# Performance work log

Hardware: AMD Instinct MI355X
Metric: run time of the kernel (lower is better)

The kernel has to match this reference:

```python
import jax, jax.numpy as jnp
import numpy as np

N, E, IN_DIM, HID, K, EXP_HID = 50000, 800000, 128, 64, 4, 64


def _xavier(key, shape):
    fan_in, fan_out = shape[-2], shape[-1]
    lim = np.sqrt(6.0 / (fan_in + fan_out)).astype(np.float32)
    return jax.random.uniform(key, shape, jnp.float32, -lim, lim)


def setup_inputs() -> dict:
    key = jax.random.key(0)
    ks = jax.random.split(key, 6)
    return {
        "x": jax.random.normal(ks[0], (N, IN_DIM), jnp.float32),
        "edge_index": jax.random.randint(ks[1], (2, E), 0, N),
        # InitDisenLayer: K per-channel Linear(IN_DIM -> HID)
        "W_init": _xavier(ks[2], (K, IN_DIM, HID)),
        "b_init": jnp.zeros((K, HID), jnp.float32),
        # elayers: Linear(2*HID -> EXP_HID) -> ReLU -> Linear(EXP_HID -> 1)
        "W1": _xavier(ks[3], (2 * HID, EXP_HID)),
        "b1": jnp.zeros((EXP_HID,), jnp.float32),
        "W2": _xavier(ks[4], (EXP_HID, 1)),
        "b2": jnp.zeros((1,), jnp.float32),
    }


def reference(x, edge_index, W_init, b_init, W1, b1, W2, b2):
    # InitDisenLayer: per-channel linear -> relu -> l2-normalize => Z [N, K, HID]
    Z = jax.nn.relu(jnp.einsum('ni,kih->nkh', x, W_init) + b_init)
    Z = Z / jnp.maximum(jnp.linalg.norm(Z, axis=-1, keepdims=True), 1e-12)

    # global_max_pool per channel over the single graph (batch == zeros) -> [K, HID]
    disen_graph_emb = jnp.max(Z, axis=0)

    # per-channel edge MLP: concat(Z[src,i], Z[dst,i]) -> Linear -> ReLU -> Linear(->1)
    # split W1 so the concat is never materialized: [E, K, 2*HID] avoided
    src, dst = edge_index[0], edge_index[1]
    W1s, W1d = W1[:HID], W1[HID:]
    h = jax.nn.relu(
        jnp.einsum('ekh,ho->eko', Z[src], W1s)
        + jnp.einsum('ekh,ho->eko', Z[dst], W1d)
        + b1
    )  # [E, K, EXP_HID]
    e = jnp.einsum('eko,o->ek', h, W2[:, 0]) + b2[0]  # [E, K]

    e_h_all = e.T                       # [K, E]
    e_h_final = jnp.max(e_h_all, axis=0)  # [E]
    return disen_graph_emb, Z, e_h_final, e_h_all
```

## Files before the change

kernel.cpp:

```cpp
#include <hip/hip_runtime.h>
#include <hip/hip_bf16.h>
#include <math.h>

#define N_NODES 50000
#define E_EDGES 800000
#define IN_DIM  128
#define HID     64
#define KF      4
#define EXP_HID 64

#define OFF_DISEN 0
#define OFF_Z     (KF*HID)
#define OFF_EHF   (OFF_Z + N_NODES*KF*HID)
#define OFF_EHALL (OFF_EHF + E_EDGES)

#define NROWS (N_NODES * KF)
#define EPW 64

typedef __bf16 bf16x8 __attribute__((ext_vector_type(8)));
typedef float  f32x4  __attribute__((ext_vector_type(4)));
typedef unsigned short ushort_t;
typedef unsigned int   uint_t;

__global__ __launch_bounds__(256) void prep_kernel(
    const float* __restrict__ W, const float* __restrict__ W1,
    float* __restrict__ disen, __bf16* __restrict__ Wz,
    __bf16* __restrict__ Wpq) {
  const int b = blockIdx.x, tid = threadIdx.x;
  if (b < 32) {
#pragma unroll
    for (int i = 0; i < 4; ++i) {
      const int idx = (b * 4 + i) * 256 + tid;
      const int k  = idx >> 13;
      const int ii = (idx >> 6) & 127;
      const int h  = idx & 63;
      const int col = k * 64 + h;
      const int t = col >> 4, c = col & 15;
      const int kh = ii >> 5, g = (ii >> 3) & 3, e = ii & 7;
      Wz[((t * 4 + kh) * 4 + g) * 128 + c * 8 + e] = (__bf16)W[idx];
    }
  } else if (b < 40) {
#pragma unroll
    for (int i = 0; i < 4; ++i) {
      const int idx = ((b - 32) * 4 + i) * 256 + tid;
      const int r = idx >> 6, cc = idx & 63;
      const int k = (r < 64) ? r : (r - 64);
      const int j = (r < 64) ? cc : (64 + cc);
      const int t = j >> 4, c = j & 15;
      const int kh = k >> 5, g = (k >> 3) & 3, e = k & 7;
      Wpq[((t * 2 + kh) * 4 + g) * 128 + c * 8 + e] = (__bf16)W1[idx];
    }
  } else {
    disen[tid] = 0.f;
  }
}

__global__ __launch_bounds__(256) void z_mfma_kernel2(
    const float* __restrict__ x, const float* __restrict__ b_init,
    const __bf16* __restrict__ Wz, float* __restrict__ out) {
  __shared__ float dred[4][256];
  const int tid = threadIdx.x;
  const int w = tid >> 6, l = tid & 63;
  const int lg = l >> 4, lc = l & 15;
  const int n0 = blockIdx.x * 64;
  const int ra = min(n0 + w * 16 + lc, N_NODES - 1);

  bf16x8 af[4];
#pragma unroll
  for (int kh = 0; kh < 4; ++kh) {
    const float4* xp = (const float4*)(x + (size_t)ra * IN_DIM + kh * 32 + lg * 8);
    const float4 f0 = xp[0], f1 = xp[1];
    bf16x8 a;
    a[0] = (__bf16)f0.x; a[1] = (__bf16)f0.y;
    a[2] = (__bf16)f0.z; a[3] = (__bf16)f0.w;
    a[4] = (__bf16)f1.x; a[5] = (__bf16)f1.y;
    a[6] = (__bf16)f1.z; a[7] = (__bf16)f1.w;
    af[kh] = a;
  }

#pragma unroll 1
  for (int k = 0; k < KF; ++k) {
    f32x4 acc[4];
#pragma unroll
    for (int tt = 0; tt < 4; ++tt) acc[tt] = (f32x4){0.f, 0.f, 0.f, 0.f};

#pragma unroll
    for (int tt = 0; tt < 4; ++tt)
#pragma unroll
      for (int kh = 0; kh < 4; ++kh) {
        const bf16x8 bf = *(const bf16x8*)(
            Wz + (((k * 4 + tt) * 4 + kh) * 4 + lg) * 128 + lc * 8);
        acc[tt] = __builtin_amdgcn_mfma_f32_16x16x32_bf16(af[kh], bf, acc[tt],
                                                          0, 0, 0);
      }

    float vals[4][4];
#pragma unroll
    for (int tt = 0; tt < 4; ++tt) {
      const float bias = b_init[(k * 4 + tt) * 16 + lc];
#pragma unroll
      for (int r = 0; r < 4; ++r)
        vals[tt][r] = fmaxf(acc[tt][r] + bias, 0.f);
    }
    float s[4];
#pragma unroll
    for (int r = 0; r < 4; ++r)
      s[r] = vals[0][r] * vals[0][r] + vals[1][r] * vals[1][r] +
             vals[2][r] * vals[2][r] + vals[3][r] * vals[3][r];
#pragma unroll
    for (int d = 1; d < 16; d <<= 1)
#pragma unroll
      for (int r = 0; r < 4; ++r) s[r] += __shfl_xor(s[r], d, 64);
    float rn[4];
#pragma unroll
    for (int r = 0; r < 4; ++r)
      rn[r] = 1.f / fmaxf(sqrtf(s[r]), 1e-12f);

#pragma unroll
    for (int tt = 0; tt < 4; ++tt) {
      const int col = k * 64 + tt * 16 + lc;
      float dmt = 0.f;
#pragma unroll
      for (int r = 0; r < 4; ++r) {
        const float zn = vals[tt][r] * rn[r];
        const int node = n0 + w * 16 + lg * 4 + r;
        if (node < N_NODES)
          out[OFF_Z + (size_t)node * (KF * HID) + col] = zn;
        dmt = fmaxf(dmt, zn);
      }
      dmt = fmaxf(dmt, __shfl_xor(dmt, 16, 64));
      dmt = fmaxf(dmt, __shfl_xor(dmt, 32, 64));
      if (lg == 0) dred[w][col] = dmt;
    }
  }
  __syncthreads();
  {
    const float m = fmaxf(fmaxf(dred[0][tid], dred[1][tid]),
                          fmaxf(dred[2][tid], dred[3][tid]));
    atomicMax((unsigned int*)(out + OFF_DISEN + tid), __float_as_uint(m));
  }
}

__global__ __launch_bounds__(256) void pq_mfma_kernel3(
    const float* __restrict__ Z, const float* __restrict__ b1,
    const __bf16* __restrict__ Wpq, unsigned char* __restrict__ P8,
    unsigned char* __restrict__ Q8, float* __restrict__ Psc,
    float* __restrict__ Qsc) {
  const int tid = threadIdx.x;
  const int w = tid >> 6, l = tid & 63;
  const int lg = l >> 4, lc = l & 15;
  const int base = blockIdx.x * 64;
  const int rowA = base + w * 16 + lc;

  bf16x8 af[2];
#pragma unroll
  for (int kh = 0; kh < 2; ++kh) {
    const float4* zp = (const float4*)(Z + (size_t)rowA * HID + kh * 32 + lg * 8);
    const float4 f0 = zp[0], f1 = zp[1];
    bf16x8 a;
    a[0] = (__bf16)f0.x; a[1] = (__bf16)f0.y;
    a[2] = (__bf16)f0.z; a[3] = (__bf16)f0.w;
    a[4] = (__bf16)f1.x; a[5] = (__bf16)f1.y;
    a[6] = (__bf16)f1.z; a[7] = (__bf16)f1.w;
    af[kh] = a;
  }

  f32x4 acc[8];
#pragma unroll
  for (int t = 0; t < 8; ++t) acc[t] = (f32x4){0.f, 0.f, 0.f, 0.f};

#pragma unroll
  for (int t = 0; t < 8; ++t)
#pragma unroll
    for (int kh = 0; kh < 2; ++kh) {
      const bf16x8 bf =
          *(const bf16x8*)(Wpq + ((t * 2 + kh) * 4 + lg) * 128 + lc * 8);
      acc[t] = __builtin_amdgcn_mfma_f32_16x16x32_bf16(af[kh], bf, acc[t],
                                                       0, 0, 0);
    }

  float pvv[4][4], qvv[4][4];
#pragma unroll
  for (int t = 0; t < 4; ++t) {
    const float bias = b1[t * 16 + lc];
#pragma unroll
    for (int r = 0; r < 4; ++r) {
      pvv[t][r] = acc[t][r] + bias;
      qvv[t][r] = acc[t + 4][r];
    }
  }

#pragma unroll
  for (int r = 0; r < 4; ++r) {
    float pm = fmaxf(fmaxf(fabsf(pvv[0][r]), fabsf(pvv[1][r])),
                     fmaxf(fabsf(pvv[2][r]), fabsf(pvv[3][r])));
    float qm = fmaxf(fmaxf(fabsf(qvv[0][r]), fabsf(qvv[1][r])),
                     fmaxf(fabsf(qvv[2][r]), fabsf(qvv[3][r])));
#pragma unroll
    for (int d = 1; d < 16; d <<= 1) {
      pm = fmaxf(pm, __shfl_xor(pm, d, 64));
      qm = fmaxf(qm, __shfl_xor(qm, d, 64));
    }
    pm = fmaxf(pm, 1e-12f);
    qm = fmaxf(qm, 1e-12f);
    const float pinv = 127.f / pm, qinv = 127.f / qm;

    uint_t packP = 0, packQ = 0;
#pragma unroll
    for (int t = 0; t < 4; ++t) {
      const int qp = __float2int_rn(pvv[t][r] * pinv) + 128;
      const int qq = __float2int_rn(qvv[t][r] * qinv) + 128;
      packP |= (uint_t)(qp & 0xff) << (8 * t);
      packQ |= (uint_t)(qq & 0xff) << (8 * t);
    }
    const int grow = base + w * 16 + lg * 4 + r;
    *(uint_t*)(P8 + (size_t)grow * 64 + lc * 4) = packP;
    *(uint_t*)(Q8 + (size_t)grow * 64 + lc * 4) = packQ;
    if (lc == 0) {
      Psc[grow] = pm * (1.f / 127.f);
      Qsc[grow] = qm * (1.f / 127.f);
    }
  }
}

__global__ __launch_bounds__(256) void edge_kernel6(
    const int* __restrict__ ei, const float* __restrict__ W2,
    const float* __restrict__ b2, const unsigned char* __restrict__ P8,
    const unsigned char* __restrict__ Q8, const float* __restrict__ Psc,
    const float* __restrict__ Qsc, float* __restrict__ ehf,
    float* __restrict__ ehall) {
  __shared__ float tile[4][KF][EPW + 1];
  const int tid = threadIdx.x;
  const int w = tid >> 6;
  const int lane = tid & 63;
  const int lc = lane & 15, lk = lane >> 4;
  const int eb = blockIdx.x * 256 + w * EPW;

  const float w2a = W2[lc],      w2b = W2[16 + lc];
  const float w2c = W2[32 + lc], w2d = W2[48 + lc];
  const float bias2 = b2[0];

  const int srcl = ei[eb + lane];
  const int dstl = ei[E_EDGES + eb + lane];

  uint_t pv[4], qv[4];
  float ps[4], qs[4];
#pragma unroll
  for (int d = 0; d < 4; ++d) {
    const int s = __shfl(srcl, d, 64);
    const int t = __shfl(dstl, d, 64);
    pv[d] = *(const uint_t*)(P8 + (size_t)s * 256 + lane * 4);
    qv[d] = *(const uint_t*)(Q8 + (size_t)t * 256 + lane * 4);
    ps[d] = Psc[s * 4 + lk];
    qs[d] = Qsc[t * 4 + lk];
  }

#pragma unroll
  for (int i = 0; i < EPW; ++i) {
    const uint_t p = pv[i & 3], q = qv[i & 3];
    const float pss = ps[i & 3], qss = qs[i & 3];
    if (i + 4 < EPW) {
      const int s = __shfl(srcl, i + 4, 64);
      const int t = __shfl(dstl, i + 4, 64);
      pv[i & 3] = *(const uint_t*)(P8 + (size_t)s * 256 + lane * 4);
      qv[i & 3] = *(const uint_t*)(Q8 + (size_t)t * 256 + lane * 4);
      ps[i & 3] = Psc[s * 4 + lk];
      qs[i & 3] = Qsc[t * 4 + lk];
    }
    const float c = -128.f * (pss + qss);

    const float p0 = (float)(p & 0xffu);
    const float p1 = (float)((p >> 8) & 0xffu);
    const float p2 = (float)((p >> 16) & 0xffu);
    const float p3 = (float)(p >> 24);
    const float q0 = (float)(q & 0xffu);
    const float q1 = (float)((q >> 8) & 0xffu);
    const float q2 = (float)((q >> 16) & 0xffu);
    const float q3 = (float)(q >> 24);

    float s4 = fmaxf(fmaf(p0, pss, fmaf(q0, qss, c)), 0.f) * w2a;
    s4 = fmaf(fmaxf(fmaf(p1, pss, fmaf(q1, qss, c)), 0.f), w2b, s4);
    s4 = fmaf(fmaxf(fmaf(p2, pss, fmaf(q2, qss, c)), 0.f), w2c, s4);
    s4 = fmaf(fmaxf(fmaf(p3, pss, fmaf(q3, qss, c)), 0.f), w2d, s4);

    s4 += __shfl_xor(s4, 1, 64);
    s4 += __shfl_xor(s4, 2, 64);
    s4 += __shfl_xor(s4, 4, 64);
    s4 += __shfl_xor(s4, 8, 64);
    if (lc == 0) tile[w][lk][i] = s4 + bias2;
  }
  __syncthreads();

  const float v0 = tile[w][0][lane];
  const float v1 = tile[w][1][lane];
  const float v2 = tile[w][2][lane];
  const float v3 = tile[w][3][lane];
  ehall[(size_t)0 * E_EDGES + eb + lane] = v0;
  ehall[(size_t)1 * E_EDGES + eb + lane] = v1;
  ehall[(size_t)2 * E_EDGES + eb + lane] = v2;
  ehall[(size_t)3 * E_EDGES + eb + lane] = v3;
  ehf[eb + lane] = fmaxf(fmaxf(v0, v1), fmaxf(v2, v3));
}

extern "C" void kernel_launch(void* const* d_in, const int* in_sizes, int n_in,
                              void* d_out, int out_size, void* d_ws,
                              size_t ws_size, hipStream_t stream) {
  const float* x      = (const float*)d_in[0];
  const int*   ei     = (const int*)  d_in[1];
  const float* W_init = (const float*)d_in[2];
  const float* b_init = (const float*)d_in[3];
  const float* W1     = (const float*)d_in[4];
  const float* b1     = (const float*)d_in[5];
  const float* W2     = (const float*)d_in[6];
  const float* b2     = (const float*)d_in[7];
  float* out = (float*)d_out;

  unsigned char* P8 = (unsigned char*)d_ws;
  unsigned char* Q8 = P8 + (size_t)NROWS * 64;
  float* Psc = (float*)(Q8 + (size_t)NROWS * 64);
  float* Qsc = Psc + NROWS;
  __bf16* Wz  = (__bf16*)(Qsc + NROWS);
  __bf16* Wpq = Wz + 32768;

  prep_kernel<<<41, 256, 0, stream>>>(W_init, W1, out + OFF_DISEN, Wz, Wpq);
  z_mfma_kernel2<<<(N_NODES + 63) / 64, 256, 0, stream>>>(
      x, b_init, Wz, out);
  pq_mfma_kernel3<<<NROWS / 64, 256, 0, stream>>>(
      out + OFF_Z, b1, Wpq, P8, Q8, Psc, Qsc);
  edge_kernel6<<<E_EDGES / 256, 256, 0, stream>>>(
      ei, W2, b2, P8, Q8, Psc, Qsc, out + OFF_EHF, out + OFF_EHALL);
}
```

Before: 133.3 us.

## Process four edges per wave iteration with 16-byte gathers in edge kernel

The edge kernel is restructured so each 16-lane group handles its own edge. Each lane gathers 16 bytes of the quantized P/Q rows with a uint4 load instead of 4 bytes, so the loop runs 16 iterations per wave instead of 64 and the cross-lane reduction drops from four shuffle steps to two. W2 is loaded with vector loads into a per-lane register table matching the new channel/column mapping. The aim is fewer, wider gather instructions and less shuffle overhead, at the cost of more registers per lane for the pipelined uint4 buffers.

After: 128.5 us. 1.04x faster.

```diff
diff --git a/kernel.cpp b/kernel.cpp
--- a/kernel.cpp
+++ b/kernel.cpp
@@ -16,6 +16,7 @@
 
 #define NROWS (N_NODES * KF)
 #define EPW 64
+#define EPIPE 4
 
 typedef __bf16 bf16x8 __attribute__((ext_vector_type(8)));
 typedef float  f32x4  __attribute__((ext_vector_type(4)));
@@ -223,7 +224,7 @@
   }
 }
 
-__global__ __launch_bounds__(256) void edge_kernel6(
+__global__ __launch_bounds__(256) void edge_kernel8(
     const int* __restrict__ ei, const float* __restrict__ W2,
     const float* __restrict__ b2, const unsigned char* __restrict__ P8,
     const unsigned char* __restrict__ Q8, const float* __restrict__ Psc,
@@ -233,61 +234,71 @@
   const int tid = threadIdx.x;
   const int w = tid >> 6;
   const int lane = tid & 63;
-  const int lc = lane & 15, lk = lane >> 4;
+  const int g = lane >> 4;
+  const int sub = lane & 15;
+  const int k = sub >> 2;
+  const int j = sub & 3;
   const int eb = blockIdx.x * 256 + w * EPW;
 
-  const float w2a = W2[lc],      w2b = W2[16 + lc];
-  const float w2c = W2[32 + lc], w2d = W2[48 + lc];
+  float w2r[4][4];
+#pragma unroll
+  for (int b = 0; b < 4; ++b) {
+    const float4 f = *(const float4*)(W2 + b * 16 + j * 4);
+    w2r[0][b] = f.x; w2r[1][b] = f.y; w2r[2][b] = f.z; w2r[3][b] = f.w;
+  }
   const float bias2 = b2[0];
 
   const int srcl = ei[eb + lane];
   const int dstl = ei[E_EDGES + eb + lane];
 
-  uint_t pv[4], qv[4];
-  float ps[4], qs[4];
-#pragma unroll
-  for (int d = 0; d < 4; ++d) {
-    const int s = __shfl(srcl, d, 64);
-    const int t = __shfl(dstl, d, 64);
-    pv[d] = *(const uint_t*)(P8 + (size_t)s * 256 + lane * 4);
-    qv[d] = *(const uint_t*)(Q8 + (size_t)t * 256 + lane * 4);
-    ps[d] = Psc[s * 4 + lk];
-    qs[d] = Qsc[t * 4 + lk];
-  }
-
-#pragma unroll
-  for (int i = 0; i < EPW; ++i) {
-    const uint_t p = pv[i & 3], q = qv[i & 3];
-    const float pss = ps[i & 3], qss = qs[i & 3];
-    if (i + 4 < EPW) {
-      const int s = __shfl(srcl, i + 4, 64);
-      const int t = __shfl(dstl, i + 4, 64);
-      pv[i & 3] = *(const uint_t*)(P8 + (size_t)s * 256 + lane * 4);
-      qv[i & 3] = *(const uint_t*)(Q8 + (size_t)t * 256 + lane * 4);
-      ps[i & 3] = Psc[s * 4 + lk];
-      qs[i & 3] = Qsc[t * 4 + lk];
+  uint4 pv[EPIPE], qv[EPIPE];
+  float ps[EPIPE], qs[EPIPE];
+#pragma unroll
+  for (int d = 0; d < EPIPE; ++d) {
+    const int s = __shfl(srcl, d * 4 + g, 64);
+    const int t = __shfl(dstl, d * 4 + g, 64);
+    pv[d] = *(const uint4*)(P8 + (size_t)s * 256 + sub * 16);
+    qv[d] = *(const uint4*)(Q8 + (size_t)t * 256 + sub * 16);
+    ps[d] = Psc[s * 4 + k];
+    qs[d] = Qsc[t * 4 + k];
+  }
+
+#pragma unroll
+  for (int i = 0; i < 16; ++i) {
+    const uint4 p = pv[i & (EPIPE - 1)];
+    const uint4 q = qv[i & (EPIPE - 1)];
+    const float pss = ps[i & (EPIPE - 1)], qss = qs[i & (EPIPE - 1)];
+    if (i + EPIPE < 16) {
+      const int s = __shfl(srcl, (i + EPIPE) * 4 + g, 64);
+      const int t = __shfl(dstl, (i + EPIPE) * 4 + g, 64);
+      pv[i & (EPIPE - 1)] = *(const uint4*)(P8 + (size_t)s * 256 + sub * 16);
+      qv[i & (EPIPE - 1)] = *(const uint4*)(Q8 + (size_t)t * 256 + sub * 16);
+      ps[i & (EPIPE - 1)] = Psc[s * 4 + k];
+      qs[i & (EPIPE - 1)] = Qsc[t * 4 + k];
     }
     const float c = -128.f * (pss + qss);
 
-    const float p0 = (float)(p & 0xffu);
-    const float p1 = (float)((p >> 8) & 0xffu);
-    const float p2 = (float)((p >> 16) & 0xffu);
-    const float p3 = (float)(p >> 24);
-    const float q0 = (float)(q & 0xffu);
-    const float q1 = (float)((q >> 8) & 0xffu);
-    const float q2 = (float)((q >> 16) & 0xffu);
-    const float q3 = (float)(q >> 24);
-
-    float s4 = fmaxf(fmaf(p0, pss, fmaf(q0, qss, c)), 0.f) * w2a;
-    s4 = fmaf(fmaxf(fmaf(p1, pss, fmaf(q1, qss, c)), 0.f), w2b, s4);
-    s4 = fmaf(fmaxf(fmaf(p2, pss, fmaf(q2, qss, c)), 0.f), w2c, s4);
-    s4 = fmaf(fmaxf(fmaf(p3, pss, fmaf(q3, qss, c)), 0.f), w2d, s4);
-
+    const uint_t pd[4] = {p.x, p.y, p.z, p.w};
+    const uint_t qd[4] = {q.x, q.y, q.z, q.w};
+    float s4 = 0.f;
+#pragma unroll
+    for (int d = 0; d < 4; ++d) {
+      const float p0 = (float)(pd[d] & 0xffu);
+      const float p1 = (float)((pd[d] >> 8) & 0xffu);
+      const float p2 = (float)((pd[d] >> 16) & 0xffu);
+      const float p3 = (float)(pd[d] >> 24);
+      const float q0 = (float)(qd[d] & 0xffu);
+      const float q1 = (float)((qd[d] >> 8) & 0xffu);
+      const float q2 = (float)((qd[d] >> 16) & 0xffu);
+      const float q3 = (float)(qd[d] >> 24);
+      s4 = fmaf(fmaxf(fmaf(p0, pss, fmaf(q0, qss, c)), 0.f), w2r[d][0], s4);
+      s4 = fmaf(fmaxf(fmaf(p1, pss, fmaf(q1, qss, c)), 0.f), w2r[d][1], s4);
+      s4 = fmaf(fmaxf(fmaf(p2, pss, fmaf(q2, qss, c)), 0.f), w2r[d][2], s4);
+      s4 = fmaf(fmaxf(fmaf(p3, pss, fmaf(q3, qss, c)), 0.f), w2r[d][3], s4);
+    }
     s4 += __shfl_xor(s4, 1, 64);
     s4 += __shfl_xor(s4, 2, 64);
-    s4 += __shfl_xor(s4, 4, 64);
-    s4 += __shfl_xor(s4, 8, 64);
-    if (lc == 0) tile[w][lk][i] = s4 + bias2;
+    if (j == 0) tile[w][k][i * 4 + g] = s4 + bias2;
   }
   __syncthreads();
 
@@ -327,6 +338,6 @@
       x, b_init, Wz, out);
   pq_mfma_kernel3<<<NROWS / 64, 256, 0, stream>>>(
       out + OFF_Z, b1, Wpq, P8, Q8, Psc, Qsc);
-  edge_kernel6<<<E_EDGES / 256, 256, 0, stream>>>(
+  edge_kernel8<<<E_EDGES / 256, 256, 0, stream>>>(
       ei, W2, b2, P8, Q8, Psc, Qsc, out + OFF_EHF, out + OFF_EHALL);
 }
```
